# Kernel tuning notes

Hardware: AMD Instinct MI355X
Metric: run time of the kernel (lower is better)

## Reference

```python
import jax, jax.numpy as jnp
import numpy as np

N_NODES = 50000
N_EDGES = 800000
D_IN, D_HID, D_OUT = 128, 512, 128


def setup_inputs() -> dict:
    key = jax.random.key(0)
    k1, k2, k3, k4, k5 = jax.random.split(key, 5)
    nh = jax.random.normal(k1, (N_NODES, D_IN), dtype=jnp.float32)
    eh = jax.random.normal(k2, (N_EDGES, D_IN), dtype=jnp.float32)
    edge_index = jax.random.randint(k3, (2, N_EDGES), 0, N_NODES, dtype=jnp.int64)
    # 2-layer GIN MLP params (Linear(128->512), relu, Linear(512->128)), bias=True
    W1 = jax.random.normal(k4, (D_IN, D_HID), dtype=jnp.float32) * (1.0 / np.sqrt(D_IN))
    b1 = jnp.zeros((D_HID,), dtype=jnp.float32)
    W2 = jax.random.normal(k5, (D_HID, D_OUT), dtype=jnp.float32) * (1.0 / np.sqrt(D_HID))
    b2 = jnp.zeros((D_OUT,), dtype=jnp.float32)
    eps = jnp.zeros((1,), dtype=jnp.float32)  # nf_eps parameter, init 0.0
    return {"nh": nh, "eh": eh, "W1": W1, "b1": b1, "W2": W2, "b2": b2,
            "eps": eps, "edge_index": edge_index}


def reference(nh, eh, W1, b1, W2, b2, eps, edge_index):
    src, dst = edge_index[0], edge_index[1]
    # gather src features, scatter-add into dst nodes: [N, D_IN]
    nz = jax.ops.segment_sum(nh[src], dst, num_segments=nh.shape[0])
    n_h = (1.0 + eps) * nh + nz  # epsilon-scaled residual
    # GIN MLP: Linear -> relu -> Linear (dropout=0, eval)
    h = jax.nn.relu(jnp.einsum("nd,dh->nh", n_h, W1) + b1)
    n_h = jnp.einsum("nh,ho->no", h, W2) + b2
    return (n_h, eh)
```

## Files before the change

### kernel.cpp

```cpp
#include <hip/hip_runtime.h>

#define N_NODES 50000
#define N_EDGES 800000
#define D_IN 128
#define D_HID 512
#define D_OUT 128

#define EH_FLOAT4 (N_EDGES * (D_IN / 4))
#define CPB 4096

#define C_PREP 400
#define C_HIST 450
#define C_SCAN 200
#define C_FILL 450
#define C_GATH 2600
#define C_GEMMF 2150

typedef __attribute__((ext_vector_type(8))) short short8v;
typedef __attribute__((ext_vector_type(4))) float f32x4;

__device__ __forceinline__ unsigned short f2bf(float f) {
    union { float f; unsigned u; } v; v.f = f;
    unsigned u = v.u;
    return (unsigned short)((u + 0x7FFFu + ((u >> 16) & 1u)) >> 16);
}
__device__ __forceinline__ float bf2f(unsigned u16) {
    union { unsigned u; float f; } v; v.u = u16 << 16;
    return v.f;
}

__device__ __forceinline__ long long interleave(long long b, long long C,
                                                long long T, long long* w) {
    long long cb = (C == 0) ? 0 : (b * C) / T;
    bool isCopy = C != 0 && ((b + 1) * C) / T > cb;
    *w = b - cb;
    return isCopy ? cb : -1;
}

__device__ __forceinline__ void copy_chunk(const float4* __restrict__ src,
                                           float4* __restrict__ dst,
                                           long long base, long long cb) {
    const f32x4* s = (const f32x4*)src;
    f32x4* d = (f32x4*)dst;
    long long o = base + cb * CPB + threadIdx.x;
#pragma unroll
    for (int i = 0; i < 16; ++i) {
        f32x4 v = __builtin_nontemporal_load(&s[o + i * 256]);
        __builtin_nontemporal_store(v, &d[o + i * 256]);
    }
}

__global__ __launch_bounds__(256) void k_prep(const float4* __restrict__ nh,
                                              const float* __restrict__ W1,
                                              const float* __restrict__ W2,
                                              uint2* __restrict__ nh16,
                                              unsigned short* __restrict__ W1T,
                                              unsigned short* __restrict__ W2T,
                                              int* __restrict__ counts,
                                              int* __restrict__ pub,
                                              const float4* __restrict__ csrc,
                                              float4* __restrict__ cdst,
                                              long long copyBase, int copyC) {
    long long w;
    const int W = 6250 + 256 + 256 + 196;
    long long cb = interleave(blockIdx.x, copyC, W + copyC, &w);
    if (cb >= 0) { copy_chunk(csrc, cdst, copyBase, cb); return; }
    int tid = threadIdx.x;
    if (w < 6250) {
        int i = (int)w * 256 + tid;
        if (i < N_NODES * (D_IN / 4)) {
            float4 a = nh[i];
            uint2 r;
            r.x = (unsigned)f2bf(a.x) | ((unsigned)f2bf(a.y) << 16);
            r.y = (unsigned)f2bf(a.z) | ((unsigned)f2bf(a.w) << 16);
            nh16[i] = r;
        }
    } else if (w < 6506) {
        int i = (int)(w - 6250) * 256 + tid;
        int n = i >> 7, k = i & 127;
        W1T[i] = f2bf(W1[k * D_HID + n]);
    } else if (w < 6762) {
        int i = (int)(w - 6506) * 256 + tid;
        int n = i >> 9, k = i & 511;
        W2T[i] = f2bf(W2[k * D_OUT + n]);
    } else {
        int i = (int)(w - 6762) * 256 + tid;
        if (i <= N_NODES) counts[i] = 0;
        if (i < 196) pub[i] = 0;
    }
}


__global__ __launch_bounds__(256) void k_hist(const int* __restrict__ ei,
                                              int* __restrict__ counts,
                                              const float4* __restrict__ csrc,
                                              float4* __restrict__ cdst,
                                              long long copyBase, int copyC) {
    long long w;
    const int W = (N_EDGES + 255) / 256;
    long long cb = interleave(blockIdx.x, copyC, W + copyC, &w);
    if (cb >= 0) { copy_chunk(csrc, cdst, copyBase, cb); return; }
    int e = (int)w * 256 + threadIdx.x;
    if (e >= N_EDGES) return;
    atomicAdd(&counts[ei[N_EDGES + e]], 1);
}

__global__ __launch_bounds__(256) void k_scan_lb(const int* __restrict__ counts,
                                                 int* __restrict__ offs,
                                                 int* __restrict__ cursors,
                                                 int* __restrict__ pub,
                                                 const float4* __restrict__ csrc,
                                                 float4* __restrict__ cdst,
                                                 long long copyBase, int copyC) {
    long long w;
    long long cb = interleave(blockIdx.x, copyC, 196 + copyC, &w);
    if (cb >= 0) { copy_chunk(csrc, cdst, copyBase, cb); return; }
    int b = (int)w;
    __shared__ int s[256];
    __shared__ int r[256];
    int tid = threadIdx.x;
    int i = b * 256 + tid;
    int v = (i < N_NODES) ? counts[i] : 0;
    s[tid] = v;
    __syncthreads();
#pragma unroll
    for (int off = 1; off < 256; off <<= 1) {
        int t = (tid >= off) ? s[tid - off] : 0;
        __syncthreads();
        if (tid >= off) s[tid] += t;
        __syncthreads();
    }
    if (tid == 255)
        __hip_atomic_store(&pub[b], s[255] + 1, __ATOMIC_RELEASE,
                           __HIP_MEMORY_SCOPE_AGENT);
    int contrib = 0;
    if (tid < b) {
        int p;
        do {
            p = __hip_atomic_load(&pub[tid], __ATOMIC_ACQUIRE,
                                  __HIP_MEMORY_SCOPE_AGENT);
        } while (p == 0);
        contrib = p - 1;
    }
    r[tid] = contrib;
    __syncthreads();
#pragma unroll
    for (int off = 128; off > 0; off >>= 1) {
        if (tid < off) r[tid] += r[tid + off];
        __syncthreads();
    }
    int prefix = r[0];
    if (i < N_NODES) {
        int o = (s[tid] - v) + prefix;
        offs[i] = o;
        cursors[i] = o;
    }
    if (b == 0 && tid == 0) offs[N_NODES] = N_EDGES;
}

__global__ __launch_bounds__(256) void k_fill(const int* __restrict__ ei,
                                              int* __restrict__ cursors,
                                              int* __restrict__ csr_src,
                                              const float4* __restrict__ csrc,
                                              float4* __restrict__ cdst,
                                              long long copyBase, int copyC) {
    long long w;
    const int W = (N_EDGES + 255) / 256;
    long long cb = interleave(blockIdx.x, copyC, W + copyC, &w);
    if (cb >= 0) { copy_chunk(csrc, cdst, copyBase, cb); return; }
    int e = (int)w * 256 + threadIdx.x;
    if (e >= N_EDGES) return;
    int dst = ei[N_EDGES + e];
    int pos = atomicAdd(&cursors[dst], 1);
    csr_src[pos] = ei[e];
}

__global__ __launch_bounds__(256) void k_gather16(const unsigned* __restrict__ nh16,
                                                  const int* __restrict__ csr_src,
                                                  const int* __restrict__ offs,
                                                  const float* __restrict__ eps,
                                                  unsigned* __restrict__ acc16,
                                                  const float4* __restrict__ csrc,
                                                  float4* __restrict__ cdst,
                                                  long long copyBase, int copyC) {
    long long w;
    const int W = (N_NODES + 3) / 4;
    long long cb = interleave(blockIdx.x, copyC, W + copyC, &w);
    if (cb >= 0) { copy_chunk(csrc, cdst, copyBase, cb); return; }
    int node = (int)w * 4 + (threadIdx.x >> 6);
    if (node >= N_NODES) return;
    int lane = threadIdx.x & 63;
    int beg = offs[node], end = offs[node + 1];
    float sx = 0.f, sy = 0.f;
    int j = beg;
    for (; j + 1 < end; j += 2) {
        unsigned v0 = nh16[(size_t)csr_src[j] * 64 + lane];
        unsigned v1 = nh16[(size_t)csr_src[j + 1] * 64 + lane];
        sx += bf2f(v0 & 0xFFFFu) + bf2f(v1 & 0xFFFFu);
        sy += bf2f(v0 >> 16) + bf2f(v1 >> 16);
    }
    if (j < end) {
        unsigned v0 = nh16[(size_t)csr_src[j] * 64 + lane];
        sx += bf2f(v0 & 0xFFFFu);
        sy += bf2f(v0 >> 16);
    }
    float sc = 1.0f + eps[0];
    unsigned m = nh16[(size_t)node * 64 + lane];
    sx += sc * bf2f(m & 0xFFFFu);
    sy += sc * bf2f(m >> 16);
    acc16[(size_t)node * 64 + lane] =
        (unsigned)f2bf(sx) | ((unsigned)f2bf(sy) << 16);
}

__global__ __launch_bounds__(256) void k_copy_eh(const float4* __restrict__ src,
                                                 float4* __restrict__ dst) {
    int i = blockIdx.x * 256 + threadIdx.x;
    if (i >= EH_FLOAT4) return;
    const f32x4* s = (const f32x4*)src;
    f32x4* d = (f32x4*)dst;
    f32x4 v = __builtin_nontemporal_load(&s[i]);
    __builtin_nontemporal_store(v, &d[i]);
}

__global__ __launch_bounds__(256, 2) void gemm_fused(
        const unsigned short* __restrict__ A,
        const unsigned short* __restrict__ W1t,
        const float* __restrict__ b1,
        const unsigned short* __restrict__ W2t,
        const float* __restrict__ b2,
        float* __restrict__ Cout,
        int M,
        const float4* __restrict__ csrc, float4* __restrict__ cdst,
        long long copyBase, int copyC, int workW) {
    long long w;
    long long cb = interleave(blockIdx.x, copyC, workW + copyC, &w);
    if (cb >= 0) { copy_chunk(csrc, cdst, copyBase, cb); return; }

    __shared__ unsigned short As[128][40];
    __shared__ unsigned short Bs[128][40];
    __shared__ unsigned short Hs[128][136];

    const int tid = threadIdx.x;
    const int m0 = (int)w * 128;
    const int wid = tid >> 6;
    const int lane = tid & 63;
    const int wr = wid >> 1;
    const int wc = wid & 1;
    const int l15 = lane & 15;
    const int kg = lane >> 4;

    f32x4 acc2[4][4];
#pragma unroll
    for (int i = 0; i < 4; ++i)
#pragma unroll
        for (int j = 0; j < 4; ++j) acc2[i][j] = (f32x4){0.f, 0.f, 0.f, 0.f};

    for (int ht = 0; ht < 4; ++ht) {
        f32x4 acc1[4][4];
#pragma unroll
        for (int i = 0; i < 4; ++i)
#pragma unroll
            for (int j = 0; j < 4; ++j) acc1[i][j] = (f32x4){0.f, 0.f, 0.f, 0.f};

        for (int ks = 0; ks < 4; ++ks) {
#pragma unroll
            for (int p = 0; p < 2; ++p) {
                int t = tid + p * 256;
                int row = t >> 2;
                int cg = t & 3;
                float4 va = make_float4(0.f, 0.f, 0.f, 0.f);
                int gr = m0 + row;
                if (gr < M)
                    va = *(const float4*)(A + (size_t)gr * D_IN + ks * 32 + cg * 8);
                *(float4*)&As[row][cg * 8] = va;
                float4 vb = *(const float4*)(W1t + (size_t)(ht * 128 + row) * D_IN
                                             + ks * 32 + cg * 8);
                *(float4*)&Bs[row][cg * 8] = vb;
            }
            __syncthreads();
            short8v a[4], bb[4];
#pragma unroll
            for (int i = 0; i < 4; ++i)
                a[i] = *(const short8v*)&As[wr * 64 + i * 16 + l15][kg * 8];
#pragma unroll
            for (int j = 0; j < 4; ++j)
                bb[j] = *(const short8v*)&Bs[wc * 64 + j * 16 + l15][kg * 8];
#pragma unroll
            for (int i = 0; i < 4; ++i)
#pragma unroll
                for (int j = 0; j < 4; ++j)
                    acc1[i][j] = __builtin_amdgcn_mfma_f32_16x16x32_bf16(
                        a[i], bb[j], acc1[i][j], 0, 0, 0);
            __syncthreads();
        }

#pragma unroll
        for (int j = 0; j < 4; ++j) {
            int lc = wc * 64 + j * 16 + l15;
            float bv = b1[ht * 128 + lc];
#pragma unroll
            for (int i = 0; i < 4; ++i)
#pragma unroll
                for (int q = 0; q < 4; ++q) {
                    float v = acc1[i][j][q] + bv;
                    Hs[wr * 64 + i * 16 + kg * 4 + q][lc] = f2bf(fmaxf(v, 0.f));
                }
        }
        __syncthreads();

#pragma unroll
        for (int ks = 0; ks < 4; ++ks) {
            short8v a[4], bb[4];
#pragma unroll
            for (int i = 0; i < 4; ++i)
                a[i] = *(const short8v*)&Hs[wr * 64 + i * 16 + l15][ks * 32 + kg * 8];
#pragma unroll
            for (int j = 0; j < 4; ++j)
                bb[j] = *(const short8v*)(W2t + (size_t)(wc * 64 + j * 16 + l15) * D_HID
                                          + ht * 128 + ks * 32 + kg * 8);
#pragma unroll
            for (int i = 0; i < 4; ++i)
#pragma unroll
                for (int j = 0; j < 4; ++j)
                    acc2[i][j] = __builtin_amdgcn_mfma_f32_16x16x32_bf16(
                        a[i], bb[j], acc2[i][j], 0, 0, 0);
        }
        __syncthreads();
    }

#pragma unroll
    for (int j = 0; j < 4; ++j) {
        int gc = wc * 64 + j * 16 + l15;
        float bv = b2[gc];
#pragma unroll
        for (int i = 0; i < 4; ++i) {
#pragma unroll
            for (int q = 0; q < 4; ++q) {
                int gr = m0 + wr * 64 + i * 16 + kg * 4 + q;
                if (gr >= M) continue;
                Cout[(size_t)gr * D_OUT + gc] = acc2[i][j][q] + bv;
            }
        }
    }
}

extern "C" void kernel_launch(void* const* d_in, const int* in_sizes, int n_in,
                              void* d_out, int out_size, void* d_ws, size_t ws_size,
                              hipStream_t stream) {
    const float* nh  = (const float*)d_in[0];
    const float* eh  = (const float*)d_in[1];
    const float* W1  = (const float*)d_in[2];
    const float* b1  = (const float*)d_in[3];
    const float* W2  = (const float*)d_in[4];
    const float* b2  = (const float*)d_in[5];
    const float* eps = (const float*)d_in[6];
    const int*   ei  = (const int*)d_in[7];

    float* out0 = (float*)d_out;
    float* out1 = out0 + (size_t)N_NODES * D_OUT;

    const size_t NEED = 36u << 20;
    bool useWs = (d_ws != nullptr) && (ws_size >= NEED);
    char* base = useWs ? (char*)d_ws : (char*)out1;

    unsigned*       nh16  = (unsigned*)(base);
    unsigned*       acc16 = (unsigned*)(base + (13u << 20));
    unsigned short* w1t   = (unsigned short*)(base + (26u << 20));
    unsigned short* w2t   = (unsigned short*)(base + (27u << 20));
    int*            ibase = (int*)(base + (28u << 20));
    int* offs    = ibase;
    int* cursors = ibase + 65536;
    int* pub     = ibase + 131072;
    int* csr_src = ibase + 262144;

    const float4* csrc = (const float4*)eh;
    float4*       cdst = (float4*)out1;

    int c0 = useWs ? C_PREP  : 0;  long long b0 = 0;
    int c1 = useWs ? C_HIST  : 0;  long long b1c = (long long)(C_PREP) * CPB;
    int c2 = useWs ? C_SCAN  : 0;  long long b2c = (long long)(C_PREP + C_HIST) * CPB;
    int c3 = useWs ? C_FILL  : 0;  long long b3c = (long long)(C_PREP + C_HIST + C_SCAN) * CPB;
    int c4 = useWs ? C_GATH  : 0;  long long b4c = (long long)(C_PREP + C_HIST + C_SCAN + C_FILL) * CPB;
    int c5 = useWs ? C_GEMMF : 0;  long long b5c = (long long)(C_PREP + C_HIST + C_SCAN + C_FILL + C_GATH) * CPB;

    k_prep<<<6958 + c0, 256, 0, stream>>>((const float4*)nh, W1, W2,
        (uint2*)nh16, w1t, w2t, cursors, pub, csrc, cdst, b0, c0);

    k_hist<<<3125 + c1, 256, 0, stream>>>(ei, cursors, csrc, cdst, b1c, c1);
    k_scan_lb<<<196 + c2, 256, 0, stream>>>(cursors, offs, cursors, pub,
                                            csrc, cdst, b2c, c2);
    k_fill<<<3125 + c3, 256, 0, stream>>>(ei, cursors, csr_src, csrc, cdst, b3c, c3);
    k_gather16<<<12500 + c4, 256, 0, stream>>>(nh16, csr_src, offs, eps, acc16,
                                               csrc, cdst, b4c, c4);

    const int WFblocks = (N_NODES + 127) / 128;
    gemm_fused<<<WFblocks + c5, 256, 0, stream>>>(
        (const unsigned short*)acc16, w1t, b1, w2t, b2, out0,
        N_NODES, csrc, cdst, b5c, c5, WFblocks);

    if (!useWs) {
        k_copy_eh<<<(EH_FLOAT4 + 255) / 256, 256, 0, stream>>>(csrc, cdst);
    }
}
```

Measured before the change: 320.8 us.

## Keep GEMM A tile in registers, unroll gather by four, rebalance copy interleave

The fused GEMM now loads each warp's A rows straight from global memory into registers once and reuses them across all four hidden tiles. W1 fragments are read directly from global memory, which removes the As/Bs shared-memory staging and its barriers. The gather loop is unrolled to four edges per iteration to keep more independent loads in flight. The copy-chunk counts interleaved into each kernel are also shifted away from the GEMM and toward the hist and fill kernels. The extra register pressure for the A fragments may lower occupancy, and uncached global W1 reads could cost bandwidth.

```diff
diff --git a/kernel.cpp b/kernel.cpp
--- a/kernel.cpp
+++ b/kernel.cpp
@@ -10,11 +10,11 @@
 #define CPB 4096
 
 #define C_PREP 400
-#define C_HIST 450
+#define C_HIST 750
 #define C_SCAN 200
-#define C_FILL 450
+#define C_FILL 750
 #define C_GATH 2600
-#define C_GEMMF 2150
+#define C_GEMMF 1550
 
 typedef __attribute__((ext_vector_type(8))) short short8v;
 typedef __attribute__((ext_vector_type(4))) float f32x4;
@@ -193,13 +193,20 @@
     int beg = offs[node], end = offs[node + 1];
     float sx = 0.f, sy = 0.f;
     int j = beg;
-    for (; j + 1 < end; j += 2) {
-        unsigned v0 = nh16[(size_t)csr_src[j] * 64 + lane];
-        unsigned v1 = nh16[(size_t)csr_src[j + 1] * 64 + lane];
-        sx += bf2f(v0 & 0xFFFFu) + bf2f(v1 & 0xFFFFu);
-        sy += bf2f(v0 >> 16) + bf2f(v1 >> 16);
-    }
-    if (j < end) {
+    for (; j + 3 < end; j += 4) {
+        int s0 = csr_src[j];
+        int s1 = csr_src[j + 1];
+        int s2 = csr_src[j + 2];
+        int s3 = csr_src[j + 3];
+        unsigned v0 = nh16[(size_t)s0 * 64 + lane];
+        unsigned v1 = nh16[(size_t)s1 * 64 + lane];
+        unsigned v2 = nh16[(size_t)s2 * 64 + lane];
+        unsigned v3 = nh16[(size_t)s3 * 64 + lane];
+        sx += bf2f(v0 & 0xFFFFu) + bf2f(v1 & 0xFFFFu) +
+              bf2f(v2 & 0xFFFFu) + bf2f(v3 & 0xFFFFu);
+        sy += bf2f(v0 >> 16) + bf2f(v1 >> 16) + bf2f(v2 >> 16) + bf2f(v3 >> 16);
+    }
+    for (; j < end; ++j) {
         unsigned v0 = nh16[(size_t)csr_src[j] * 64 + lane];
         sx += bf2f(v0 & 0xFFFFu);
         sy += bf2f(v0 >> 16);
@@ -236,8 +243,6 @@
     long long cb = interleave(blockIdx.x, copyC, workW + copyC, &w);
     if (cb >= 0) { copy_chunk(csrc, cdst, copyBase, cb); return; }
 
-    __shared__ unsigned short As[128][40];
-    __shared__ unsigned short Bs[128][40];
     __shared__ unsigned short Hs[128][136];
 
     const int tid = threadIdx.x;
@@ -249,6 +254,22 @@
     const int l15 = lane & 15;
     const int kg = lane >> 4;
 
+    short8v af[4][4];
+#pragma unroll
+    for (int i = 0; i < 4; ++i) {
+        int gr = m0 + wr * 64 + i * 16 + l15;
+        const unsigned short* Ar = A + (size_t)gr * D_IN + kg * 8;
+        if (gr < M) {
+#pragma unroll
+            for (int ks = 0; ks < 4; ++ks)
+                af[ks][i] = *(const short8v*)(Ar + ks * 32);
+        } else {
+#pragma unroll
+            for (int ks = 0; ks < 4; ++ks)
+                af[ks][i] = (short8v){0, 0, 0, 0, 0, 0, 0, 0};
+        }
+    }
+
     f32x4 acc2[4][4];
 #pragma unroll
     for (int i = 0; i < 4; ++i)
@@ -256,53 +277,29 @@
         for (int j = 0; j < 4; ++j) acc2[i][j] = (f32x4){0.f, 0.f, 0.f, 0.f};
 
     for (int ht = 0; ht < 4; ++ht) {
-        f32x4 acc1[4][4];
-#pragma unroll
-        for (int i = 0; i < 4; ++i)
-#pragma unroll
-            for (int j = 0; j < 4; ++j) acc1[i][j] = (f32x4){0.f, 0.f, 0.f, 0.f};
-
-        for (int ks = 0; ks < 4; ++ks) {
-#pragma unroll
-            for (int p = 0; p < 2; ++p) {
-                int t = tid + p * 256;
-                int row = t >> 2;
-                int cg = t & 3;
-                float4 va = make_float4(0.f, 0.f, 0.f, 0.f);
-                int gr = m0 + row;
-                if (gr < M)
-                    va = *(const float4*)(A + (size_t)gr * D_IN + ks * 32 + cg * 8);
-                *(float4*)&As[row][cg * 8] = va;
-                float4 vb = *(const float4*)(W1t + (size_t)(ht * 128 + row) * D_IN
-                                             + ks * 32 + cg * 8);
-                *(float4*)&Bs[row][cg * 8] = vb;
+        __syncthreads();
+
+#pragma unroll
+        for (int j = 0; j < 4; ++j) {
+            const int lc = wc * 64 + j * 16 + l15;
+            const unsigned short* Wr = W1t + (size_t)(ht * 128 + lc) * D_IN + kg * 8;
+            f32x4 a1[4];
+#pragma unroll
+            for (int i = 0; i < 4; ++i) a1[i] = (f32x4){0.f, 0.f, 0.f, 0.f};
+#pragma unroll
+            for (int ks = 0; ks < 4; ++ks) {
+                short8v bbj = *(const short8v*)(Wr + ks * 32);
+#pragma unroll
+                for (int i = 0; i < 4; ++i)
+                    a1[i] = __builtin_amdgcn_mfma_f32_16x16x32_bf16(
+                        af[ks][i], bbj, a1[i], 0, 0, 0);
             }
-            __syncthreads();
-            short8v a[4], bb[4];
+            float bv = b1[ht * 128 + lc];
 #pragma unroll
             for (int i = 0; i < 4; ++i)
-                a[i] = *(const short8v*)&As[wr * 64 + i * 16 + l15][kg * 8];
-#pragma unroll
-            for (int j = 0; j < 4; ++j)
-                bb[j] = *(const short8v*)&Bs[wc * 64 + j * 16 + l15][kg * 8];
-#pragma unroll
-            for (int i = 0; i < 4; ++i)
-#pragma unroll
-                for (int j = 0; j < 4; ++j)
-                    acc1[i][j] = __builtin_amdgcn_mfma_f32_16x16x32_bf16(
-                        a[i], bb[j], acc1[i][j], 0, 0, 0);
-            __syncthreads();
-        }
-
-#pragma unroll
-        for (int j = 0; j < 4; ++j) {
-            int lc = wc * 64 + j * 16 + l15;
-            float bv = b1[ht * 128 + lc];
-#pragma unroll
-            for (int i = 0; i < 4; ++i)
 #pragma unroll
                 for (int q = 0; q < 4; ++q) {
-                    float v = acc1[i][j][q] + bv;
+                    float v = a1[i][q] + bv;
                     Hs[wr * 64 + i * 16 + kg * 4 + q][lc] = f2bf(fmaxf(v, 0.f));
                 }
         }
@@ -310,10 +307,10 @@
 
 #pragma unroll
         for (int ks = 0; ks < 4; ++ks) {
-            short8v a[4], bb[4];
+            short8v ha[4], bb[4];
 #pragma unroll
             for (int i = 0; i < 4; ++i)
-                a[i] = *(const short8v*)&Hs[wr * 64 + i * 16 + l15][ks * 32 + kg * 8];
+                ha[i] = *(const short8v*)&Hs[wr * 64 + i * 16 + l15][ks * 32 + kg * 8];
 #pragma unroll
             for (int j = 0; j < 4; ++j)
                 bb[j] = *(const short8v*)(W2t + (size_t)(wc * 64 + j * 16 + l15) * D_HID
@@ -323,9 +320,8 @@
 #pragma unroll
                 for (int j = 0; j < 4; ++j)
                     acc2[i][j] = __builtin_amdgcn_mfma_f32_16x16x32_bf16(
-                        a[i], bb[j], acc2[i][j], 0, 0, 0);
+                        ha[i], bb[j], acc2[i][j], 0, 0, 0);
         }
-        __syncthreads();
     }
 
 #pragma unroll
```

After: 301.5 us (median of 2 runs). 1.06x faster.
